# Kernel optimization log

Hardware: AMD Instinct MI355X
Metric: run time of the kernel (lower is better)

The kernel has to match this reference:

```python
import jax, jax.numpy as jnp
import numpy as np

# Module config (from init_kwargs): causal=False, window_size=(256,256), window_type=0,
# softmax_scale=None -> 1/sqrt(D), dropout=0 (eval mode).
WINDOW_LEFT, WINDOW_RIGHT = 256, 256


def _window_mask(Sq, Sk, causal, use_window_mask):
    """Boolean [Sq, Sk] visibility mask, FA2 semantics (right-aligned offset)."""
    qi = jnp.arange(Sq)[:, None]
    kj = jnp.arange(Sk)[None, :]
    offset = Sk - Sq
    if causal:
        return kj <= qi + offset  # window (-1, 0)
    if use_window_mask:
        m = jnp.ones((Sq, Sk), dtype=bool)
        if WINDOW_LEFT >= 0:
            m = m & (kj >= qi + offset - WINDOW_LEFT)
        if WINDOW_RIGHT >= 0:
            m = m & (kj <= qi + offset + WINDOW_RIGHT)
        return m
    return None  # full attention


def setup_inputs() -> dict:
    key = jax.random.key(0)
    kq, kkv = jax.random.split(key)
    B, Sq, Sk, H, D = 2, 2048, 2048, 16, 64
    q = jax.random.normal(kq, (B, Sq, H, D), dtype=jnp.float32)
    kv = jax.random.normal(kkv, (B, Sk, 2, H, D), dtype=jnp.float32)
    return {"q": q, "kv": kv, "causal": 0, "use_window_mask": 1, "return_attn_probs": 0}


def reference(q, kv, causal, use_window_mask, return_attn_probs):
    # q: (B, Sq, H, D); kv: (B, Sk, 2, H, D)
    B, Sq, H, D = q.shape
    Sk = kv.shape[1]
    k = kv[:, :, 0]  # (B, Sk, H, D)
    v = kv[:, :, 1]
    scale = 1.0 / (D ** 0.5)
    scores = jnp.einsum('bqhd,bkhd->bhqk', q, k) * scale  # (B, H, Sq, Sk)
    mask = _window_mask(Sq, Sk, bool(causal), bool(use_window_mask))
    if mask is not None:
        scores = jnp.where(mask[None, None], scores, jnp.finfo(scores.dtype).min)
    probs = jax.nn.softmax(scores, axis=-1)
    out = jnp.einsum('bhqk,bkhd->bqhd', probs, v)  # (B, Sq, H, D)
    return out
```

## Files before the change

kernel.cpp:

```cpp
#include <hip/hip_runtime.h>
#include <hip/hip_bf16.h>

#define B_    2
#define SQ_   2048
#define SK_   2048
#define NH_   16
#define DH_   64
#define WIN_  256
#define NEG_  -30000.0f

typedef __bf16 bf16_t;
typedef bf16_t bf16x8 __attribute__((ext_vector_type(8)));
typedef bf16_t bf16x4 __attribute__((ext_vector_type(4)));
typedef float  f32x4  __attribute__((ext_vector_type(4)));
typedef short  s16x4  __attribute__((ext_vector_type(4)));
typedef unsigned int u32;

#define KE_BH 131072
#define VT_E  4194304

#define GLOAD_LDS16(g, l)                                                      \
  __builtin_amdgcn_global_load_lds(                                            \
      (const __attribute__((address_space(1))) u32*)(g),                       \
      (__attribute__((address_space(3))) u32*)(l), 16, 0, 0)

__global__ __launch_bounds__(256)
void kv_prep(const float* __restrict__ kvg, bf16_t* __restrict__ wse) {
  const int t   = blockIdx.x * 256 + threadIdx.x;
  const int c   = t & 7;
  const int key = (t >> 3) & (SK_ - 1);
  const int bh  = t >> 14;
  const int b   = bh >> 4, h = bh & 15;

  const size_t base =
      ((((size_t)b * SK_ + key) * 2) * NH_ + h) * (size_t)DH_ + (size_t)(c * 8);

  {
    f32x4 a0 = *(const f32x4*)(kvg + base);
    f32x4 a1 = *(const f32x4*)(kvg + base + 4);
    bf16x8 w;
#pragma unroll
    for (int i = 0; i < 4; ++i) { w[i] = (bf16_t)a0[i]; w[i + 4] = (bf16_t)a1[i]; }
    *(bf16x8*)(wse + (size_t)bh * KE_BH + key * 64 + ((c ^ (key & 7)) << 3)) = w;
  }
  {
    const float* vsrc = kvg + base + NH_ * DH_;
    const int g = key >> 3, kw = key & 7, gh = g & ~7, gl = g & 7;
    bf16_t* vdst = wse + VT_E + (size_t)bh * KE_BH + kw;
#pragma unroll
    for (int j = 0; j < 8; ++j) {
      const int d = c * 8 + j;
      vdst[(size_t)d * 2048 + ((gh | (gl ^ j)) << 3)] = (bf16_t)vsrc[j];
    }
  }
}

__global__ __launch_bounds__(256, 4)
void fa_fwd(const float* __restrict__ qg, const bf16_t* __restrict__ wse,
            float* __restrict__ outg) {
  const int tid  = threadIdx.x;
  const int wid  = tid >> 6;
  const int lane = tid & 63;
  const int quad = lane >> 4;
  const int li   = lane & 15;
  const int lk   = li & 7;

  const int bid = blockIdx.x;
  const int qb  = bid >> 5;
  const int bh  = bid & 31;
  const int b   = bh >> 4;
  const int h   = bh & 15;

  const int q0b = qb * 64;
  const int q0  = q0b + wid * 16;

  __shared__ __align__(16) bf16_t sK[2][4096];
  __shared__ __align__(16) bf16_t sV[2][4096];

  const bf16_t* kbh = wse + (size_t)bh * KE_BH;
  const bf16_t* vbh = wse + VT_E + (size_t)bh * KE_BH;

  const float qscale = 0.125f * 1.44269504088896340736f;
  const float* qrow = qg + ((size_t)((b * SQ_ + q0 + li) * NH_ + h)) * DH_;
  bf16x8 qfrag[2];
#pragma unroll
  for (int c = 0; c < 2; ++c) {
    f32x4 a0 = *(const f32x4*)(qrow + c * 32 + quad * 8);
    f32x4 a1 = *(const f32x4*)(qrow + c * 32 + quad * 8 + 4);
#pragma unroll
    for (int i = 0; i < 4; ++i) {
      qfrag[c][i]     = (bf16_t)(a0[i] * qscale);
      qfrag[c][i + 4] = (bf16_t)(a1[i] * qscale);
    }
  }

  f32x4 oacc[4];
#pragma unroll
  for (int t = 0; t < 4; ++t) { f32x4 z = {0.f, 0.f, 0.f, 0.f}; oacc[t] = z; }
  float m = NEG_, l = 0.f;

  int klo = q0b - WIN_; if (klo < 0) klo = 0;
  int khi = q0b + 63 + WIN_ + 1; if (khi > SK_) khi = SK_;
  const int nt = (khi - klo + 63) >> 6;

  const int tid8 = tid * 8;
  const int vs0  = (tid >> 3) * 2048 + (tid & 7) * 8;

  GLOAD_LDS16(kbh + klo * 64 + tid8,        &sK[0][tid8]);
  GLOAD_LDS16(kbh + klo * 64 + 2048 + tid8, &sK[0][2048 + tid8]);
  GLOAD_LDS16(vbh + klo + vs0,              &sV[0][tid8]);
  GLOAD_LDS16(vbh + klo + vs0 + 65536,      &sV[0][2048 + tid8]);
  __syncthreads();

  int buf = 0;
  for (int t = 0; t < nt; ++t) {
    const int kk = klo + t * 64;
    if (t + 1 < nt) {
      const int kn = kk + 64;
      GLOAD_LDS16(kbh + kn * 64 + tid8,        &sK[buf ^ 1][tid8]);
      GLOAD_LDS16(kbh + kn * 64 + 2048 + tid8, &sK[buf ^ 1][2048 + tid8]);
      GLOAD_LDS16(vbh + kn + vs0,              &sV[buf ^ 1][tid8]);
      GLOAD_LDS16(vbh + kn + vs0 + 65536,      &sV[buf ^ 1][2048 + tid8]);
    }

    if (kk + 63 >= q0 - WIN_ && kk <= q0 + 15 + WIN_) {
      f32x4 sc[4];
      __builtin_amdgcn_s_setprio(1);
#pragma unroll
      for (int s = 0; s < 4; ++s) {
        const int row = (s * 16 + li) * 64;
        bf16x8 kf0 = *(const bf16x8*)(&sK[buf][row + ((quad ^ lk) << 3)]);
        bf16x8 kf1 = *(const bf16x8*)(&sK[buf][row + (((quad + 4) ^ lk) << 3)]);
        f32x4 acc = {0.f, 0.f, 0.f, 0.f};
        acc = __builtin_amdgcn_mfma_f32_16x16x32_bf16(kf0, qfrag[0], acc, 0, 0, 0);
        acc = __builtin_amdgcn_mfma_f32_16x16x32_bf16(kf1, qfrag[1], acc, 0, 0, 0);
        sc[s] = acc;
      }
      __builtin_amdgcn_s_setprio(0);

      if (kk < q0 - 241 || kk > q0 + 193) {
        const int qa = q0 + li;
#pragma unroll
        for (int s = 0; s < 4; ++s)
#pragma unroll
          for (int r = 0; r < 4; ++r) {
            int key = kk + s * 16 + quad * 4 + r;
            unsigned dd = (unsigned)(key - qa + WIN_);
            if (dd > 2u * WIN_) sc[s][r] = NEG_;
          }
      }
      float tl = NEG_;
#pragma unroll
      for (int s = 0; s < 4; ++s)
        tl = fmaxf(tl, fmaxf(fmaxf(sc[s][0], sc[s][1]), fmaxf(sc[s][2], sc[s][3])));

      const bool defer = (__all(tl <= m + 8.0f) != 0);
      float mnew = m;
      if (!defer) {
        float tr = fmaxf(tl, __shfl_xor(tl, 16));
        tr = fmaxf(tr, __shfl_xor(tr, 32));
        mnew = fmaxf(m, tr);
      }

      float psum = 0.f;
      bf16x4 pa[4];
#pragma unroll
      for (int s = 0; s < 4; ++s) {
        float p0 = exp2f(sc[s][0] - mnew);
        float p1 = exp2f(sc[s][1] - mnew);
        float p2 = exp2f(sc[s][2] - mnew);
        float p3 = exp2f(sc[s][3] - mnew);
        psum += (p0 + p1) + (p2 + p3);
        pa[s][0] = (bf16_t)p0; pa[s][1] = (bf16_t)p1;
        pa[s][2] = (bf16_t)p2; pa[s][3] = (bf16_t)p3;
      }

      if (!defer) {
        const float alpha = exp2f(m - mnew);
        float al[4];
#pragma unroll
        for (int r = 0; r < 4; ++r) al[r] = __shfl(alpha, quad * 4 + r);
#pragma unroll
        for (int t2 = 0; t2 < 4; ++t2) {
          oacc[t2][0] *= al[0]; oacc[t2][1] *= al[1];
          oacc[t2][2] *= al[2]; oacc[t2][3] *= al[3];
        }
        l = l * alpha + psum;
        m = mnew;
      } else {
        l += psum;
      }

      __builtin_amdgcn_s_setprio(1);
#pragma unroll
      for (int s = 0; s < 4; ++s) {
        const s16x4 pas = __builtin_bit_cast(s16x4, pa[s]);
        const int cA = 2 * s + (quad >> 1);
#pragma unroll
        for (int t2 = 0; t2 < 4; ++t2) {
          const int d = 16 * t2 + li;
          s16x4 vb = *(const s16x4*)(
              &sV[buf][d * 64 + ((cA ^ lk) << 3) + (quad & 1) * 4]);
          oacc[t2] = __builtin_amdgcn_mfma_f32_16x16x16bf16_1k(pas, vb, oacc[t2], 0, 0, 0);
        }
      }
      __builtin_amdgcn_s_setprio(0);
    }

    __syncthreads();
    buf ^= 1;
  }

  l += __shfl_xor(l, 16);
  l += __shfl_xor(l, 32);
  float rl[4];
#pragma unroll
  for (int r = 0; r < 4; ++r) {
    float lv = __shfl(l, quad * 4 + r);
    rl[r] = 1.0f / lv;
  }
  float* orow = outg + ((size_t)((b * SQ_ + q0) * NH_ + h)) * DH_;
#pragma unroll
  for (int t = 0; t < 4; ++t)
#pragma unroll
    for (int r = 0; r < 4; ++r)
      orow[(size_t)(quad * 4 + r) * (NH_ * DH_) + 16 * t + li] = oacc[t][r] * rl[r];
}

extern "C" void kernel_launch(void* const* d_in, const int* in_sizes, int n_in,
                              void* d_out, int out_size, void* d_ws, size_t ws_size,
                              hipStream_t stream) {
  (void)in_sizes; (void)n_in; (void)out_size; (void)ws_size;
  const float* q  = (const float*)d_in[0];
  const float* kv = (const float*)d_in[1];
  float* out = (float*)d_out;
  bf16_t* wse = (bf16_t*)d_ws;

  kv_prep<<<dim3(2048), 256, 0, stream>>>(kv, wse);
  fa_fwd<<<dim3(B_ * NH_ * (SQ_ / 64)), 256, 0, stream>>>(q, wse, out);
}
```

Measured before the change: 125.8 us.

## Triple-buffer K/V tiles with explicit waitcnt and transpose V through LDS in prep

The attention kernel moves from double to triple buffering of the K/V LDS tiles, prefetching two tiles ahead and replacing __syncthreads with explicit vmcnt/lgkmcnt waits plus a raw barrier, so global loads overlap more of the compute. The kv_prep kernel now transposes V through shared memory and writes it with coalesced 16-byte stores instead of scattered 2-byte stores. The extra LDS per block lowers the occupancy hint from 4 to 3 blocks, and the hand-written waitcnt logic depends on the counts of outstanding loads being exact.

```diff
diff --git a/kernel.cpp b/kernel.cpp
--- a/kernel.cpp
+++ b/kernel.cpp
@@ -26,36 +26,52 @@
 
 __global__ __launch_bounds__(256)
 void kv_prep(const float* __restrict__ kvg, bf16_t* __restrict__ wse) {
-  const int t   = blockIdx.x * 256 + threadIdx.x;
-  const int c   = t & 7;
-  const int key = (t >> 3) & (SK_ - 1);
-  const int bh  = t >> 14;
+  __shared__ __align__(16) bf16_t sT[4096];
+  const int tid = threadIdx.x;
+  const int bb  = blockIdx.x;
+  const int bh  = bb >> 5, kt = bb & 31;
   const int b   = bh >> 4, h = bh & 15;
 
-  const size_t base =
-      ((((size_t)b * SK_ + key) * 2) * NH_ + h) * (size_t)DH_ + (size_t)(c * 8);
-
-  {
-    f32x4 a0 = *(const f32x4*)(kvg + base);
-    f32x4 a1 = *(const f32x4*)(kvg + base + 4);
+  const int skey = tid >> 2;
+  const int sd0  = (tid & 3) * 16;
+  const int key  = kt * 64 + skey;
+
+  const float* src =
+      kvg + ((((size_t)b * SK_ + key) * 2) * NH_ + h) * (size_t)DH_ + sd0;
+  f32x4 ka[4], va[4];
+#pragma unroll
+  for (int i = 0; i < 4; ++i) {
+    ka[i] = *(const f32x4*)(src + 4 * i);
+    va[i] = *(const f32x4*)(src + NH_ * DH_ + 4 * i);
+  }
+
+  bf16_t* kdst = wse + (size_t)bh * KE_BH + (size_t)key * 64;
+#pragma unroll
+  for (int hh = 0; hh < 2; ++hh) {
     bf16x8 w;
 #pragma unroll
-    for (int i = 0; i < 4; ++i) { w[i] = (bf16_t)a0[i]; w[i + 4] = (bf16_t)a1[i]; }
-    *(bf16x8*)(wse + (size_t)bh * KE_BH + key * 64 + ((c ^ (key & 7)) << 3)) = w;
-  }
-  {
-    const float* vsrc = kvg + base + NH_ * DH_;
-    const int g = key >> 3, kw = key & 7, gh = g & ~7, gl = g & 7;
-    bf16_t* vdst = wse + VT_E + (size_t)bh * KE_BH + kw;
-#pragma unroll
-    for (int j = 0; j < 8; ++j) {
-      const int d = c * 8 + j;
-      vdst[(size_t)d * 2048 + ((gh | (gl ^ j)) << 3)] = (bf16_t)vsrc[j];
-    }
-  }
+    for (int i = 0; i < 4; ++i) {
+      w[i] = (bf16_t)ka[2 * hh][i]; w[i + 4] = (bf16_t)ka[2 * hh + 1][i];
+    }
+    const int c = (sd0 >> 3) + hh;
+    *(bf16x8*)(kdst + ((c ^ (key & 7)) << 3)) = w;
+  }
+
+  const int g = skey >> 3, kw = skey & 7;
+#pragma unroll
+  for (int j = 0; j < 16; ++j) {
+    const int d = sd0 + j;
+    sT[d * 64 + ((g ^ (d & 7)) << 3) + kw] = (bf16_t)va[j >> 2][j & 3];
+  }
+  __syncthreads();
+
+  const int dr = tid >> 2, rp = (tid & 3) * 16;
+  bf16_t* vdst = wse + VT_E + (size_t)bh * KE_BH + (size_t)dr * 2048 + kt * 64 + rp;
+  *(bf16x8*)(vdst)     = *(const bf16x8*)(&sT[dr * 64 + rp]);
+  *(bf16x8*)(vdst + 8) = *(const bf16x8*)(&sT[dr * 64 + rp + 8]);
 }
 
-__global__ __launch_bounds__(256, 4)
+__global__ __launch_bounds__(256, 3)
 void fa_fwd(const float* __restrict__ qg, const bf16_t* __restrict__ wse,
             float* __restrict__ outg) {
   const int tid  = threadIdx.x;
@@ -74,8 +90,8 @@
   const int q0b = qb * 64;
   const int q0  = q0b + wid * 16;
 
-  __shared__ __align__(16) bf16_t sK[2][4096];
-  __shared__ __align__(16) bf16_t sV[2][4096];
+  __shared__ __align__(16) bf16_t sK[3][4096];
+  __shared__ __align__(16) bf16_t sV[3][4096];
 
   const bf16_t* kbh = wse + (size_t)bh * KE_BH;
   const bf16_t* vbh = wse + VT_E + (size_t)bh * KE_BH;
@@ -106,22 +122,25 @@
   const int tid8 = tid * 8;
   const int vs0  = (tid >> 3) * 2048 + (tid & 7) * 8;
 
-  GLOAD_LDS16(kbh + klo * 64 + tid8,        &sK[0][tid8]);
-  GLOAD_LDS16(kbh + klo * 64 + 2048 + tid8, &sK[0][2048 + tid8]);
-  GLOAD_LDS16(vbh + klo + vs0,              &sV[0][tid8]);
-  GLOAD_LDS16(vbh + klo + vs0 + 65536,      &sV[0][2048 + tid8]);
-  __syncthreads();
-
-  int buf = 0;
+  bf16_t* k0 = sK[0]; bf16_t* k1 = sK[1]; bf16_t* k2 = sK[2];
+  bf16_t* v0 = sV[0]; bf16_t* v1 = sV[1]; bf16_t* v2 = sV[2];
+
+  auto stage_async = [&](int kt, bf16_t* kd, bf16_t* vd) {
+    GLOAD_LDS16(kbh + kt * 64 + tid8,        kd + tid8);
+    GLOAD_LDS16(kbh + kt * 64 + 2048 + tid8, kd + 2048 + tid8);
+    GLOAD_LDS16(vbh + kt + vs0,              vd + tid8);
+    GLOAD_LDS16(vbh + kt + vs0 + 65536,      vd + 2048 + tid8);
+  };
+
+  stage_async(klo, k0, v0);
+  stage_async(klo + 64, k1, v1);
+  asm volatile("s_waitcnt vmcnt(4)" ::: "memory");
+  __builtin_amdgcn_s_barrier();
+  __builtin_amdgcn_sched_barrier(0);
+
   for (int t = 0; t < nt; ++t) {
     const int kk = klo + t * 64;
-    if (t + 1 < nt) {
-      const int kn = kk + 64;
-      GLOAD_LDS16(kbh + kn * 64 + tid8,        &sK[buf ^ 1][tid8]);
-      GLOAD_LDS16(kbh + kn * 64 + 2048 + tid8, &sK[buf ^ 1][2048 + tid8]);
-      GLOAD_LDS16(vbh + kn + vs0,              &sV[buf ^ 1][tid8]);
-      GLOAD_LDS16(vbh + kn + vs0 + 65536,      &sV[buf ^ 1][2048 + tid8]);
-    }
+    if (t + 2 < nt) stage_async(klo + (t + 2) * 64, k2, v2);
 
     if (kk + 63 >= q0 - WIN_ && kk <= q0 + 15 + WIN_) {
       f32x4 sc[4];
@@ -129,8 +148,8 @@
 #pragma unroll
       for (int s = 0; s < 4; ++s) {
         const int row = (s * 16 + li) * 64;
-        bf16x8 kf0 = *(const bf16x8*)(&sK[buf][row + ((quad ^ lk) << 3)]);
-        bf16x8 kf1 = *(const bf16x8*)(&sK[buf][row + (((quad + 4) ^ lk) << 3)]);
+        bf16x8 kf0 = *(const bf16x8*)(&k0[row + ((quad ^ lk) << 3)]);
+        bf16x8 kf1 = *(const bf16x8*)(&k0[row + (((quad + 4) ^ lk) << 3)]);
         f32x4 acc = {0.f, 0.f, 0.f, 0.f};
         acc = __builtin_amdgcn_mfma_f32_16x16x32_bf16(kf0, qfrag[0], acc, 0, 0, 0);
         acc = __builtin_amdgcn_mfma_f32_16x16x32_bf16(kf1, qfrag[1], acc, 0, 0, 0);
@@ -200,15 +219,22 @@
         for (int t2 = 0; t2 < 4; ++t2) {
           const int d = 16 * t2 + li;
           s16x4 vb = *(const s16x4*)(
-              &sV[buf][d * 64 + ((cA ^ lk) << 3) + (quad & 1) * 4]);
+              &v0[d * 64 + ((cA ^ lk) << 3) + (quad & 1) * 4]);
           oacc[t2] = __builtin_amdgcn_mfma_f32_16x16x16bf16_1k(pas, vb, oacc[t2], 0, 0, 0);
         }
       }
       __builtin_amdgcn_s_setprio(0);
     }
 
-    __syncthreads();
-    buf ^= 1;
+    if (t + 1 < nt) {
+      asm volatile("s_waitcnt lgkmcnt(0)" ::: "memory");
+      if (t + 2 < nt) asm volatile("s_waitcnt vmcnt(4)" ::: "memory");
+      else            asm volatile("s_waitcnt vmcnt(0)" ::: "memory");
+      __builtin_amdgcn_s_barrier();
+      __builtin_amdgcn_sched_barrier(0);
+    }
+    bf16_t* tk = k0; k0 = k1; k1 = k2; k2 = tk;
+    bf16_t* tv = v0; v0 = v1; v1 = v2; v2 = tv;
   }
 
   l += __shfl_xor(l, 16);
@@ -236,6 +262,6 @@
   float* out = (float*)d_out;
   bf16_t* wse = (bf16_t*)d_ws;
 
-  kv_prep<<<dim3(2048), 256, 0, stream>>>(kv, wse);
+  kv_prep<<<dim3(32 * 32), 256, 0, stream>>>(kv, wse);
   fa_fwd<<<dim3(B_ * NH_ * (SQ_ / 64)), 256, 0, stream>>>(q, wse, out);
 }
```

New measurement: 123.0 us. -2.2%, faster.
